# Kernel tuning notes

Measured on AMD Instinct MI355X. Metric: run time of the kernel, lower is better.

## Reference

```python
import jax, jax.numpy as jnp
import numpy as np

B, T, H, N = 4, 2048, 1024, 16
DT_MIN, DT_MAX = 1e-3, 1e-1
A_INIT_MIN, A_INIT_MAX = 0.5, 2.0


def _inv_softplus(x):
    # log(exp(x) - 1), numerically stable
    return x + jnp.log(-jnp.expm1(-x))


def setup_inputs() -> dict:
    key = jax.random.key(0)
    kx, ka, kb, kc, kw, kdt = jax.random.split(key, 6)
    x = jax.random.normal(kx, (B, T, H), dtype=jnp.float32)
    A_log = jax.random.uniform(ka, (H, N), minval=np.log(A_INIT_MIN), maxval=np.log(A_INIT_MAX), dtype=jnp.float32)
    B_mat = 0.02 * jax.random.normal(kb, (H, N), dtype=jnp.float32)
    C_mat = 0.02 * jax.random.normal(kc, (H, N), dtype=jnp.float32)
    D_vec = jnp.ones((H,), dtype=jnp.float32)
    W_dt = 0.02 * jax.random.normal(kw, (H, H), dtype=jnp.float32)
    b_dt = _inv_softplus(jax.random.uniform(kdt, (H,), minval=DT_MIN, maxval=DT_MAX, dtype=jnp.float32))
    return {"x": x, "A_log": A_log, "B_mat": B_mat, "C_mat": C_mat, "D_vec": D_vec, "W_dt": W_dt, "b_dt": b_dt}


def reference(x, A_log, B_mat, C_mat, D_vec, W_dt, b_dt):
    # in_proj is Identity since input_size == hidden_size
    u = x  # (B, T, H)
    A = -jnp.exp(A_log)  # (H, N)
    # dt for all timesteps at once: softplus(u @ W_dt^T + b_dt) -> (B, T, H)
    dt = jax.nn.softplus(jnp.einsum('bth,gh->btg', u, W_dt) + b_dt)
    state0 = jnp.zeros((u.shape[0], A_log.shape[0], A_log.shape[1]), dtype=u.dtype)

    def step(state, inp):
        dt_t, u_t = inp  # (B, H), (B, H)
        dtA = dt_t[..., None]  # (B, H, 1)
        A_bar = jnp.exp(dtA * A)                       # (B, H, N)
        state = A_bar * state + (dtA * B_mat) * u_t[..., None]
        y_t = jnp.einsum('bhn,hn->bh', state, C_mat) + D_vec * u_t
        return state, y_t

    # scan over time axis
    state_final, ys = jax.lax.scan(step, state0, (dt.transpose(1, 0, 2), u.transpose(1, 0, 2)))
    out = ys.transpose(1, 0, 2)  # (B, T, H)
    return out, state_final
```

## Files before the change

### kernel.cpp

```cpp
#include <hip/hip_runtime.h>
#include <stdint.h>

#define BB 4
#define TT 2048
#define HH 1024
#define NN 16
#define KK 1024
#define GG 1024
#define MM (BB*TT)
#define NCHUNK 64
#define TC (TT/NCHUNK)
#define HB 256

#if __has_builtin(__builtin_amdgcn_exp2f)
#define FAST_EXP2(x) __builtin_amdgcn_exp2f(x)
#else
#define FAST_EXP2(x) __expf((x) * 0.6931471805599453f)
#endif
#define EXPSCALE 1.4426950408889634f

typedef __attribute__((ext_vector_type(8))) short short8;
typedef __attribute__((ext_vector_type(4))) float f32x4;

__device__ __forceinline__ unsigned short f2bf(float f) {
  union { float f; unsigned u; } a; a.f = f;
  unsigned u = a.u;
  u += 0x7fffu + ((u >> 16) & 1u);
  return (unsigned short)(u >> 16);
}

__global__ __launch_bounds__(256) void cvt2_f32_bf16(const float* __restrict__ srcA,
                                                     unsigned short* __restrict__ dstA, int n4a,
                                                     const float* __restrict__ srcB,
                                                     unsigned short* __restrict__ dstB, int n4b) {
  int i = blockIdx.x * blockDim.x + threadIdx.x;
  const float* s; unsigned short* d; int j;
  if (i < n4a) { s = srcA; d = dstA; j = i; }
  else         { s = srcB; d = dstB; j = i - n4a; if (j >= n4b) return; }
  float4 a = ((const float4*)s)[j];
  ushort4 o;
  o.x = f2bf(a.x); o.y = f2bf(a.y); o.z = f2bf(a.z); o.w = f2bf(a.w);
  ((ushort4*)d)[j] = o;
}

__global__ __launch_bounds__(256) void gemm_dt(const unsigned short* __restrict__ xb,
                                               const unsigned short* __restrict__ wb,
                                               const float* __restrict__ b_dt,
                                               _Float16* __restrict__ dtH) {
  __shared__ short lsA[128 * 32];
  __shared__ short lsB[64 * 32];
  const int tid  = threadIdx.x;
  const int w    = tid >> 6;
  const int lane = tid & 63;
  const int bid  = blockIdx.x;
  const int swz  = (bid & 7) * 128 + (bid >> 3);
  const int m0 = (swz >> 4) * 128;
  const int g0 = (swz & 15) * 64;

  const int ea  = w * 1024 + lane * 8;
  const int am0 = ea >> 5,         ak0 = ea & 31;
  const int am1 = (ea + 512) >> 5, ak1 = (ea + 512) & 31;
  const int eb  = w * 512 + lane * 8;
  const int bg0 = eb >> 5,         bk0 = eb & 31;
  const unsigned short* gA0 = xb + (size_t)(m0 + am0) * KK + ak0;
  const unsigned short* gA1 = xb + (size_t)(m0 + am1) * KK + ak1;
  const unsigned short* gB0 = wb + (size_t)(g0 + bg0) * KK + bk0;
  short* lA0 = lsA + w * 1024;
  short* lB0 = lsB + w * 512;

  const int wm   = (w >> 1) * 64;
  const int wg   = (w & 1) * 32;
  const int lrow = lane & 15;
  const int lq   = lane >> 4;

  f32x4 acc[4][2];
  const f32x4 zero = {0.f, 0.f, 0.f, 0.f};
#pragma unroll
  for (int i = 0; i < 4; ++i)
#pragma unroll
    for (int j = 0; j < 2; ++j) acc[i][j] = zero;

  for (int kt = 0; kt < KK / 32; ++kt) {
    const int ko = kt * 32;
    __builtin_amdgcn_global_load_lds((__attribute__((address_space(1))) void*)(gA0 + ko),
                                     (__attribute__((address_space(3))) void*)(lA0), 16, 0, 0);
    __builtin_amdgcn_global_load_lds((__attribute__((address_space(1))) void*)(gA1 + ko),
                                     (__attribute__((address_space(3))) void*)(lA0 + 512), 16, 0, 0);
    __builtin_amdgcn_global_load_lds((__attribute__((address_space(1))) void*)(gB0 + ko),
                                     (__attribute__((address_space(3))) void*)(lB0), 16, 0, 0);
    __syncthreads();

    short8 af[4], bfr[2];
#pragma unroll
    for (int mi = 0; mi < 4; ++mi)
      af[mi] = *(const short8*)&lsA[(wm + mi * 16 + lrow) * 32 + lq * 8];
#pragma unroll
    for (int ni = 0; ni < 2; ++ni)
      bfr[ni] = *(const short8*)&lsB[(wg + ni * 16 + lrow) * 32 + lq * 8];
#pragma unroll
    for (int mi = 0; mi < 4; ++mi)
#pragma unroll
      for (int ni = 0; ni < 2; ++ni)
        acc[mi][ni] = __builtin_amdgcn_mfma_f32_16x16x32_bf16(af[mi], bfr[ni], acc[mi][ni], 0, 0, 0);
    __syncthreads();
  }

  const int mrow = m0 + wm + lq * 4;
#pragma unroll
  for (int ni = 0; ni < 2; ++ni) {
    const int g = g0 + wg + ni * 16 + lrow;
    const float bias = b_dt[g];
#pragma unroll
    for (int mi = 0; mi < 4; ++mi)
#pragma unroll
      for (int r = 0; r < 4; ++r) {
        float z = acc[mi][ni][r] + bias;
        dtH[(size_t)(mrow + mi * 16 + r) * GG + g] =
            (_Float16)(fmaxf(z, 0.f) + __logf(1.f + __expf(-fabsf(z))));
      }
  }
}

__global__ __launch_bounds__(256, 4) void ssm_phase1(const float* __restrict__ x,
                                                     const _Float16* __restrict__ dtH,
                                                     const float* __restrict__ A_log,
                                                     float* __restrict__ sloc,
                                                     float* __restrict__ sdArr) {
  const int tid = threadIdx.x;
  const int bid = blockIdx.x;
  const int hb = bid & (HH / HB - 1);
  const int b  = (bid >> 2) & (BB - 1);
  const int c  = bid >> 4;
  const int h  = hb * HB + tid;

  const size_t base = ((size_t)b * TT + c * TC) * HH + h;
  const float*    up = x + base;
  const _Float16* dp = dtH + base;

  float Ae[NN];
#pragma unroll
  for (int n = 0; n < NN; ++n) Ae[n] = -__expf(A_log[h * NN + n]) * EXPSCALE;

  float s[NN];
#pragma unroll
  for (int n = 0; n < NN; ++n) s[n] = 0.f;
  float sd = 0.f;

#pragma unroll
  for (int j = 0; j < TC / 8; ++j) {
    float uu[8], dv[8];
#pragma unroll
    for (int i = 0; i < 8; ++i) {
      uu[i] = up[(size_t)(j * 8 + i) * HH];
      dv[i] = (float)dp[(size_t)(j * 8 + i) * HH];
    }
#pragma unroll
    for (int i = 0; i < 8; ++i) {
      const float dtv = dv[i];
      const float du  = dtv * uu[i];
      sd += dtv;
#pragma unroll
      for (int n = 0; n < NN; ++n) {
        const float ab = FAST_EXP2(dtv * Ae[n]);
        s[n] = fmaf(ab, s[n], du);
      }
    }
  }

  float* sp = sloc + (((size_t)c * BB + b) * HH + h) * NN;
#pragma unroll
  for (int n = 0; n < NN; n += 4) {
    f32x4 v = {s[n], s[n + 1], s[n + 2], s[n + 3]};
    *(f32x4*)&sp[n] = v;
  }
  sdArr[((size_t)c * BB + b) * HH + h] = sd;
}

__global__ __launch_bounds__(256) void ssm_phase2(float* __restrict__ sloc,
                                                  const float* __restrict__ sdArr,
                                                  const float* __restrict__ A_log,
                                                  const float* __restrict__ Bm_,
                                                  float* __restrict__ stateOut) {
  const int id = blockIdx.x * 256 + threadIdx.x;
  const int hn = id & (HH * NN - 1);
  const int bh = id >> 4;
  const float Ae = -__expf(A_log[hn]) * EXPSCALE;
  float carry = 0.f;
#pragma unroll 4
  for (int ch = 0; ch < NCHUNK; ++ch) {
    const size_t idx = (size_t)ch * (BB * HH * NN) + id;
    const float sl = sloc[idx];
    const float dc = FAST_EXP2(Ae * sdArr[(size_t)ch * (BB * HH) + bh]);
    sloc[idx] = carry;
    carry = fmaf(dc, carry, sl);
  }
  stateOut[id] = Bm_[hn] * carry;
}

__global__ __launch_bounds__(256, 4) void ssm_phase3(const float* __restrict__ x,
                                                     const _Float16* __restrict__ dtH,
                                                     const float* __restrict__ A_log,
                                                     const float* __restrict__ Bm_,
                                                     const float* __restrict__ Cm_,
                                                     const float* __restrict__ Dv_,
                                                     const float* __restrict__ carryBuf,
                                                     float* __restrict__ out) {
  const int tid = threadIdx.x;
  const int bid = blockIdx.x;
  const int hb = bid & (HH / HB - 1);
  const int b  = (bid >> 2) & (BB - 1);
  const int c  = bid >> 4;
  const int h  = hb * HB + tid;

  const size_t base = ((size_t)b * TT + c * TC) * HH + h;
  const float*    up = x + base;
  const _Float16* dp = dtH + base;
  float*          yo = out + base;

  float Ae[NN], Cb[NN];
#pragma unroll
  for (int n = 0; n < NN; ++n) {
    Ae[n] = -__expf(A_log[h * NN + n]) * EXPSCALE;
    Cb[n] = Cm_[h * NN + n] * Bm_[h * NN + n];
  }
  const float Dv = Dv_[h];

  float s[NN];
  const float* cp = carryBuf + (((size_t)c * BB + b) * HH + h) * NN;
#pragma unroll
  for (int n = 0; n < NN; n += 4) {
    f32x4 v = *(const f32x4*)&cp[n];
    s[n] = v[0]; s[n + 1] = v[1]; s[n + 2] = v[2]; s[n + 3] = v[3];
  }

#pragma unroll
  for (int j = 0; j < TC / 8; ++j) {
    float uu[8], dv[8];
#pragma unroll
    for (int i = 0; i < 8; ++i) {
      uu[i] = up[(size_t)(j * 8 + i) * HH];
      dv[i] = (float)dp[(size_t)(j * 8 + i) * HH];
    }
#pragma unroll
    for (int i = 0; i < 8; ++i) {
      const float dtv = dv[i];
      const float uv  = uu[i];
      const float du  = dtv * uv;
      float y0 = Dv * uv, y1 = 0.f, y2 = 0.f, y3 = 0.f;
#pragma unroll
      for (int n = 0; n < NN; n += 4) {
        float ab;
        ab = FAST_EXP2(dtv * Ae[n]);     s[n]     = fmaf(ab, s[n],     du); y0 = fmaf(Cb[n],     s[n],     y0);
        ab = FAST_EXP2(dtv * Ae[n + 1]); s[n + 1] = fmaf(ab, s[n + 1], du); y1 = fmaf(Cb[n + 1], s[n + 1], y1);
        ab = FAST_EXP2(dtv * Ae[n + 2]); s[n + 2] = fmaf(ab, s[n + 2], du); y2 = fmaf(Cb[n + 2], s[n + 2], y2);
        ab = FAST_EXP2(dtv * Ae[n + 3]); s[n + 3] = fmaf(ab, s[n + 3], du); y3 = fmaf(Cb[n + 3], s[n + 3], y3);
      }
      yo[(size_t)(j * 8 + i) * HH] = (y0 + y1) + (y2 + y3);
    }
  }
}

extern "C" void kernel_launch(void* const* d_in, const int* in_sizes, int n_in,
                              void* d_out, int out_size, void* d_ws, size_t ws_size,
                              hipStream_t stream) {
  const float* x     = (const float*)d_in[0];
  const float* A_log = (const float*)d_in[1];
  const float* B_mat = (const float*)d_in[2];
  const float* C_mat = (const float*)d_in[3];
  const float* D_vec = (const float*)d_in[4];
  const float* W_dt  = (const float*)d_in[5];
  const float* b_dt  = (const float*)d_in[6];
  float* out = (float*)d_out;

  char* ws = (char*)d_ws;
  unsigned short* xb  = (unsigned short*)(ws);
  unsigned short* wb  = (unsigned short*)(ws + 16777216);
  _Float16*       dtH = (_Float16*)(ws + 18874368);
  float*          sloc  = (float*)(ws);
  float*          sdArr = (float*)(ws + 16777216);
  float* stateOut = out + (size_t)BB * TT * HH;

  const int n4x = MM * KK / 4, n4w = GG * KK / 4;
  cvt2_f32_bf16<<<(n4x + n4w + 255) / 256, 256, 0, stream>>>(x, xb, n4x, W_dt, wb, n4w);
  gemm_dt<<<(MM / 128) * (GG / 64), 256, 0, stream>>>(xb, wb, b_dt, dtH);

  const int nblk = (HH / HB) * BB * NCHUNK;
  ssm_phase1<<<nblk, 256, 0, stream>>>(x, dtH, A_log, sloc, sdArr);
  ssm_phase2<<<(BB * HH * NN) / 256, 256, 0, stream>>>(sloc, sdArr, A_log, B_mat, stateOut);
  ssm_phase3<<<nblk, 256, 0, stream>>>(x, dtH, A_log, B_mat, C_mat, D_vec, sloc, out);
}
```

Before: 183.4 us.

## Compute local y in phase1, apply carry correction in phase3; widen GEMM tile

Phase1 now also computes the chunk-local output (zero initial state) and the cumulative dt sum. It stores both as a packed half2 per element, so phase3 no longer re-runs the recurrence. Phase3 only adds the carry contribution C·B·carry·exp(A·cumsum dt), which replaces the state update with an exp plus FMA. It reads one 4-byte word instead of x and dt. The GEMM tile for dt is widened from 128x64 to 128x128 per block for more MFMA reuse per LDS load. The trade-off is fp16 precision for local y and cumulative dt, plus an extra 32MB workspace write/read.

```diff
diff --git a/kernel.cpp b/kernel.cpp
--- a/kernel.cpp
+++ b/kernel.cpp
@@ -27,6 +27,12 @@
   unsigned u = a.u;
   u += 0x7fffu + ((u >> 16) & 1u);
   return (unsigned short)(u >> 16);
+}
+
+__device__ __forceinline__ unsigned pack_half2(float a, float b) {
+  union { _Float16 h[2]; unsigned u; } p;
+  p.h[0] = (_Float16)a; p.h[1] = (_Float16)b;
+  return p.u;
 }
 
 __global__ __launch_bounds__(256) void cvt2_f32_bf16(const float* __restrict__ srcA,
@@ -48,37 +54,36 @@
                                                const float* __restrict__ b_dt,
                                                _Float16* __restrict__ dtH) {
   __shared__ short lsA[128 * 32];
-  __shared__ short lsB[64 * 32];
+  __shared__ short lsB[128 * 32];
   const int tid  = threadIdx.x;
   const int w    = tid >> 6;
   const int lane = tid & 63;
   const int bid  = blockIdx.x;
-  const int swz  = (bid & 7) * 128 + (bid >> 3);
-  const int m0 = (swz >> 4) * 128;
-  const int g0 = (swz & 15) * 64;
+  const int swz  = (bid & 7) * 64 + (bid >> 3);
+  const int m0 = (swz >> 3) * 128;
+  const int g0 = (swz & 7) * 128;
 
   const int ea  = w * 1024 + lane * 8;
   const int am0 = ea >> 5,         ak0 = ea & 31;
   const int am1 = (ea + 512) >> 5, ak1 = (ea + 512) & 31;
-  const int eb  = w * 512 + lane * 8;
-  const int bg0 = eb >> 5,         bk0 = eb & 31;
   const unsigned short* gA0 = xb + (size_t)(m0 + am0) * KK + ak0;
   const unsigned short* gA1 = xb + (size_t)(m0 + am1) * KK + ak1;
-  const unsigned short* gB0 = wb + (size_t)(g0 + bg0) * KK + bk0;
+  const unsigned short* gB0 = wb + (size_t)(g0 + am0) * KK + ak0;
+  const unsigned short* gB1 = wb + (size_t)(g0 + am1) * KK + ak1;
   short* lA0 = lsA + w * 1024;
-  short* lB0 = lsB + w * 512;
+  short* lB0 = lsB + w * 1024;
 
   const int wm   = (w >> 1) * 64;
-  const int wg   = (w & 1) * 32;
+  const int wn   = (w & 1) * 64;
   const int lrow = lane & 15;
   const int lq   = lane >> 4;
 
-  f32x4 acc[4][2];
+  f32x4 acc[4][4];
   const f32x4 zero = {0.f, 0.f, 0.f, 0.f};
 #pragma unroll
   for (int i = 0; i < 4; ++i)
 #pragma unroll
-    for (int j = 0; j < 2; ++j) acc[i][j] = zero;
+    for (int j = 0; j < 4; ++j) acc[i][j] = zero;
 
   for (int kt = 0; kt < KK / 32; ++kt) {
     const int ko = kt * 32;
@@ -88,27 +93,29 @@
                                      (__attribute__((address_space(3))) void*)(lA0 + 512), 16, 0, 0);
     __builtin_amdgcn_global_load_lds((__attribute__((address_space(1))) void*)(gB0 + ko),
                                      (__attribute__((address_space(3))) void*)(lB0), 16, 0, 0);
+    __builtin_amdgcn_global_load_lds((__attribute__((address_space(1))) void*)(gB1 + ko),
+                                     (__attribute__((address_space(3))) void*)(lB0 + 512), 16, 0, 0);
     __syncthreads();
 
-    short8 af[4], bfr[2];
+    short8 af[4], bfr[4];
 #pragma unroll
     for (int mi = 0; mi < 4; ++mi)
       af[mi] = *(const short8*)&lsA[(wm + mi * 16 + lrow) * 32 + lq * 8];
 #pragma unroll
-    for (int ni = 0; ni < 2; ++ni)
-      bfr[ni] = *(const short8*)&lsB[(wg + ni * 16 + lrow) * 32 + lq * 8];
+    for (int ni = 0; ni < 4; ++ni)
+      bfr[ni] = *(const short8*)&lsB[(wn + ni * 16 + lrow) * 32 + lq * 8];
 #pragma unroll
     for (int mi = 0; mi < 4; ++mi)
 #pragma unroll
-      for (int ni = 0; ni < 2; ++ni)
+      for (int ni = 0; ni < 4; ++ni)
         acc[mi][ni] = __builtin_amdgcn_mfma_f32_16x16x32_bf16(af[mi], bfr[ni], acc[mi][ni], 0, 0, 0);
     __syncthreads();
   }
 
   const int mrow = m0 + wm + lq * 4;
 #pragma unroll
-  for (int ni = 0; ni < 2; ++ni) {
-    const int g = g0 + wg + ni * 16 + lrow;
+  for (int ni = 0; ni < 4; ++ni) {
+    const int g = g0 + wn + ni * 16 + lrow;
     const float bias = b_dt[g];
 #pragma unroll
     for (int mi = 0; mi < 4; ++mi)
@@ -124,8 +131,12 @@
 __global__ __launch_bounds__(256, 4) void ssm_phase1(const float* __restrict__ x,
                                                      const _Float16* __restrict__ dtH,
                                                      const float* __restrict__ A_log,
+                                                     const float* __restrict__ Bm_,
+                                                     const float* __restrict__ Cm_,
+                                                     const float* __restrict__ Dv_,
                                                      float* __restrict__ sloc,
-                                                     float* __restrict__ sdArr) {
+                                                     float* __restrict__ sdArr,
+                                                     unsigned* __restrict__ ylsd) {
   const int tid = threadIdx.x;
   const int bid = blockIdx.x;
   const int hb = bid & (HH / HB - 1);
@@ -136,10 +147,15 @@
   const size_t base = ((size_t)b * TT + c * TC) * HH + h;
   const float*    up = x + base;
   const _Float16* dp = dtH + base;
-
-  float Ae[NN];
-#pragma unroll
-  for (int n = 0; n < NN; ++n) Ae[n] = -__expf(A_log[h * NN + n]) * EXPSCALE;
+  unsigned*       yp = ylsd + base;
+
+  float Ae[NN], Cb[NN];
+#pragma unroll
+  for (int n = 0; n < NN; ++n) {
+    Ae[n] = -__expf(A_log[h * NN + n]) * EXPSCALE;
+    Cb[n] = Cm_[h * NN + n] * Bm_[h * NN + n];
+  }
+  const float Dv = Dv_[h];
 
   float s[NN];
 #pragma unroll
@@ -157,13 +173,19 @@
 #pragma unroll
     for (int i = 0; i < 8; ++i) {
       const float dtv = dv[i];
-      const float du  = dtv * uu[i];
+      const float uv  = uu[i];
+      const float du  = dtv * uv;
       sd += dtv;
-#pragma unroll
-      for (int n = 0; n < NN; ++n) {
-        const float ab = FAST_EXP2(dtv * Ae[n]);
-        s[n] = fmaf(ab, s[n], du);
+      float y0 = Dv * uv, y1 = 0.f, y2 = 0.f, y3 = 0.f;
+#pragma unroll
+      for (int n = 0; n < NN; n += 4) {
+        float ab;
+        ab = FAST_EXP2(dtv * Ae[n]);     s[n]     = fmaf(ab, s[n],     du); y0 = fmaf(Cb[n],     s[n],     y0);
+        ab = FAST_EXP2(dtv * Ae[n + 1]); s[n + 1] = fmaf(ab, s[n + 1], du); y1 = fmaf(Cb[n + 1], s[n + 1], y1);
+        ab = FAST_EXP2(dtv * Ae[n + 2]); s[n + 2] = fmaf(ab, s[n + 2], du); y2 = fmaf(Cb[n + 2], s[n + 2], y2);
+        ab = FAST_EXP2(dtv * Ae[n + 3]); s[n + 3] = fmaf(ab, s[n + 3], du); y3 = fmaf(Cb[n + 3], s[n + 3], y3);
       }
+      yp[(size_t)(j * 8 + i) * HH] = pack_half2((y0 + y1) + (y2 + y3), sd);
     }
   }
 
@@ -197,12 +219,10 @@
   stateOut[id] = Bm_[hn] * carry;
 }
 
-__global__ __launch_bounds__(256, 4) void ssm_phase3(const float* __restrict__ x,
-                                                     const _Float16* __restrict__ dtH,
+__global__ __launch_bounds__(256, 4) void ssm_phase3(const unsigned* __restrict__ ylsd,
                                                      const float* __restrict__ A_log,
                                                      const float* __restrict__ Bm_,
                                                      const float* __restrict__ Cm_,
-                                                     const float* __restrict__ Dv_,
                                                      const float* __restrict__ carryBuf,
                                                      float* __restrict__ out) {
   const int tid = threadIdx.x;
@@ -213,47 +233,38 @@
   const int h  = hb * HB + tid;
 
   const size_t base = ((size_t)b * TT + c * TC) * HH + h;
-  const float*    up = x + base;
-  const _Float16* dp = dtH + base;
+  const unsigned* yp = ylsd + base;
   float*          yo = out + base;
 
-  float Ae[NN], Cb[NN];
-#pragma unroll
-  for (int n = 0; n < NN; ++n) {
-    Ae[n] = -__expf(A_log[h * NN + n]) * EXPSCALE;
-    Cb[n] = Cm_[h * NN + n] * Bm_[h * NN + n];
-  }
-  const float Dv = Dv_[h];
-
-  float s[NN];
+  float Ae[NN], cc[NN];
+#pragma unroll
+  for (int n = 0; n < NN; ++n) Ae[n] = -__expf(A_log[h * NN + n]) * EXPSCALE;
+
   const float* cp = carryBuf + (((size_t)c * BB + b) * HH + h) * NN;
 #pragma unroll
   for (int n = 0; n < NN; n += 4) {
     f32x4 v = *(const f32x4*)&cp[n];
-    s[n] = v[0]; s[n + 1] = v[1]; s[n + 2] = v[2]; s[n + 3] = v[3];
+#pragma unroll
+    for (int q = 0; q < 4; ++q)
+      cc[n + q] = Cm_[h * NN + n + q] * Bm_[h * NN + n + q] * v[q];
   }
 
 #pragma unroll
   for (int j = 0; j < TC / 8; ++j) {
-    float uu[8], dv[8];
+    unsigned vv[8];
+#pragma unroll
+    for (int i = 0; i < 8; ++i) vv[i] = yp[(size_t)(j * 8 + i) * HH];
 #pragma unroll
     for (int i = 0; i < 8; ++i) {
-      uu[i] = up[(size_t)(j * 8 + i) * HH];
-      dv[i] = (float)dp[(size_t)(j * 8 + i) * HH];
-    }
-#pragma unroll
-    for (int i = 0; i < 8; ++i) {
-      const float dtv = dv[i];
-      const float uv  = uu[i];
-      const float du  = dtv * uv;
-      float y0 = Dv * uv, y1 = 0.f, y2 = 0.f, y3 = 0.f;
+      union { unsigned u; _Float16 hh[2]; } q; q.u = vv[i];
+      const float sdv = (float)q.hh[1];
+      float y0 = (float)q.hh[0], y1 = 0.f, y2 = 0.f, y3 = 0.f;
 #pragma unroll
       for (int n = 0; n < NN; n += 4) {
-        float ab;
-        ab = FAST_EXP2(dtv * Ae[n]);     s[n]     = fmaf(ab, s[n],     du); y0 = fmaf(Cb[n],     s[n],     y0);
-        ab = FAST_EXP2(dtv * Ae[n + 1]); s[n + 1] = fmaf(ab, s[n + 1], du); y1 = fmaf(Cb[n + 1], s[n + 1], y1);
-        ab = FAST_EXP2(dtv * Ae[n + 2]); s[n + 2] = fmaf(ab, s[n + 2], du); y2 = fmaf(Cb[n + 2], s[n + 2], y2);
-        ab = FAST_EXP2(dtv * Ae[n + 3]); s[n + 3] = fmaf(ab, s[n + 3], du); y3 = fmaf(Cb[n + 3], s[n + 3], y3);
+        y0 = fmaf(cc[n],     FAST_EXP2(Ae[n]     * sdv), y0);
+        y1 = fmaf(cc[n + 1], FAST_EXP2(Ae[n + 1] * sdv), y1);
+        y2 = fmaf(cc[n + 2], FAST_EXP2(Ae[n + 2] * sdv), y2);
+        y3 = fmaf(cc[n + 3], FAST_EXP2(Ae[n + 3] * sdv), y3);
       }
       yo[(size_t)(j * 8 + i) * HH] = (y0 + y1) + (y2 + y3);
     }
@@ -273,19 +284,20 @@
   float* out = (float*)d_out;
 
   char* ws = (char*)d_ws;
-  unsigned short* xb  = (unsigned short*)(ws);
-  unsigned short* wb  = (unsigned short*)(ws + 16777216);
-  _Float16*       dtH = (_Float16*)(ws + 18874368);
+  unsigned short* xb   = (unsigned short*)(ws);
+  unsigned short* wb   = (unsigned short*)(ws + 16777216);
+  _Float16*       dtH  = (_Float16*)(ws + 18874368);
+  unsigned*       ylsd = (unsigned*)(ws + 35651584);
   float*          sloc  = (float*)(ws);
   float*          sdArr = (float*)(ws + 16777216);
   float* stateOut = out + (size_t)BB * TT * HH;
 
   const int n4x = MM * KK / 4, n4w = GG * KK / 4;
   cvt2_f32_bf16<<<(n4x + n4w + 255) / 256, 256, 0, stream>>>(x, xb, n4x, W_dt, wb, n4w);
-  gemm_dt<<<(MM / 128) * (GG / 64), 256, 0, stream>>>(xb, wb, b_dt, dtH);
+  gemm_dt<<<(MM / 128) * (GG / 128), 256, 0, stream>>>(xb, wb, b_dt, dtH);
 
   const int nblk = (HH / HB) * BB * NCHUNK;
-  ssm_phase1<<<nblk, 256, 0, stream>>>(x, dtH, A_log, sloc, sdArr);
+  ssm_phase1<<<nblk, 256, 0, stream>>>(x, dtH, A_log, B_mat, C_mat, D_vec, sloc, sdArr, ylsd);
   ssm_phase2<<<(BB * HH * NN) / 256, 256, 0, stream>>>(sloc, sdArr, A_log, B_mat, stateOut);
-  ssm_phase3<<<nblk, 256, 0, stream>>>(x, dtH, A_log, B_mat, C_mat, D_vec, sloc, out);
-}
+  ssm_phase3<<<nblk, 256, 0, stream>>>(ylsd, A_log, B_mat, C_mat, sloc, out);
+}
```

After: 189.1 us. 3.1% more time.
